# Kernel optimization log

Hardware: AMD Instinct MI355X
Metric: run time of the kernel (lower is better)

Reference implementation:

```python
import jax, jax.numpy as jnp
import numpy as np

INFTY_APPROX = 1e+30
ROTARY_BASE = 10000.0
D_HEAD = 128


def rope(x):
    # x: [B, H, T, D]
    *_, length, width = x.shape
    half = width // 2
    positions = jnp.arange(length)[:, None].astype(x.dtype)          # [T, 1]
    dims = jnp.arange(half).astype(x.dtype)                           # [half]
    ang_freqs = jnp.power(ROTARY_BASE, -dims / half)[None, :]         # [1, half]
    radians = positions * ang_freqs                                   # [T, half]
    cos = jnp.cos(radians)[None, None].astype(x.dtype)                # [1,1,T,half]
    sin = jnp.sin(radians)[None, None].astype(x.dtype)
    even, odd = jnp.split(x, 2, axis=-1)
    r_even = even * cos - odd * sin
    r_odd = even * sin + odd * cos
    return jnp.concatenate([r_even, r_odd], axis=-1)


def setup_inputs() -> dict:
    key = jax.random.key(0)
    ks = jax.random.split(key, 5)
    B, T, M, D = 4, 2048, 1024, D_HEAD
    H = M // D
    x = jax.random.normal(ks[0], (B, T, M), dtype=jnp.float32)
    scale = M ** -0.5
    wq = jax.random.normal(ks[1], (H, M, D), dtype=jnp.float32) * scale
    wk = jax.random.normal(ks[2], (H, M, D), dtype=jnp.float32) * scale
    wv = jax.random.normal(ks[3], (H, M, D), dtype=jnp.float32) * scale
    wo = jax.random.normal(ks[4], (H, D, M), dtype=jnp.float32) * scale
    return {"x": x, "wq": wq, "wk": wk, "wv": wv, "wo": wo}


def reference(x, wq, wk, wv, wo):
    # x: [B, T, M]; w{q,k,v}: [H, M, D]; wo: [H, D, M]
    q = jnp.einsum('bim,hmd->bhid', x, wq)
    k = jnp.einsum('bim,hmd->bhid', x, wk)
    v = jnp.einsum('bim,hmd->bhid', x, wv)
    q = rope(q)
    k = rope(k)
    # NOTE: module scales BOTH q and k by d_head**-0.5 (mup-style 1/d overall)
    mult = jnp.asarray(D_HEAD ** -0.5, dtype=x.dtype)
    s = jnp.einsum('bhid,bhjd->bhij', q * mult, k * mult)
    T = s.shape[-1]
    i = jnp.arange(T)[:, None]
    j = jnp.arange(T)[None, :]
    mask = (i < j).astype(s.dtype)[None, None]  # future positions masked
    s = s - jnp.asarray(INFTY_APPROX, dtype=s.dtype) * mask
    p = jax.nn.softmax(s, axis=-1)
    o = jnp.einsum('bhij,bhjd->bhid', p, v)
    r = jnp.einsum('bhid,hdm->bim', o, wo)
    return r
```

## Files before the change

### kernel.cpp

```cpp
#include <hip/hip_runtime.h>
#include <math.h>


typedef unsigned short u16;
typedef __attribute__((ext_vector_type(8))) short short8;
typedef __attribute__((ext_vector_type(4))) float floatx4;

#define MFMA_B16(a, b, c) __builtin_amdgcn_mfma_f32_16x16x32_bf16((a), (b), (c), 0, 0, 0)

__device__ __forceinline__ void async_cp16(const void* g, void* l) {
  __builtin_amdgcn_global_load_lds(
      (const __attribute__((address_space(1))) unsigned int*)g,
      (__attribute__((address_space(3))) unsigned int*)l, 16, 0, 0);
}

__device__ __forceinline__ u16 f2bf(float f) {
  unsigned u = __float_as_uint(f);
  u += 0x7FFFu + ((u >> 16) & 1u);
  return (u16)(u >> 16);
}

__device__ __forceinline__ unsigned cvt_pk_bf16(float lo, float hi) {
  unsigned r;
  asm("v_cvt_pk_bf16_f32 %0, %1, %2" : "=v"(r) : "v"(lo), "v"(hi));
  return r;
}

__device__ __forceinline__ int swz8(int row, int chunk) { return ((chunk ^ (row & 7)) << 3); }

__global__ void prep_all(const float* __restrict__ x, const float* __restrict__ wq,
                         const float* __restrict__ wk, const float* __restrict__ wv,
                         const float* __restrict__ wo, u16* __restrict__ xb,
                         u16* __restrict__ wT, u16* __restrict__ woT,
                         float2* __restrict__ tab) {
  __shared__ float tile[32][33];
  const int bid = blockIdx.x;
  const int tid = threadIdx.x;

  if (bid < 8192) {
    int idx = (bid * 256 + tid) * 4;
    float4 v = *(const float4*)(x + idx);
    ushort4 o = make_ushort4(f2bf(v.x), f2bf(v.y), f2bf(v.z), f2bf(v.w));
    *(ushort4*)(xb + idx) = o;
  } else if (bid < 11264) {
    int id2 = bid - 8192;
    int z = id2 >> 10;
    int rem = id2 & 1023;
    int by = rem >> 5, bx = rem & 31;
    const float* src = (z == 0) ? wq : (z == 1) ? wk : wv;
    u16* dst = wT + (size_t)z * 1024 * 1024;
    int h = by >> 2, dt = by & 3;
    int m0 = bx * 32, d0 = dt * 32;
    int tx = tid & 31, ty = tid >> 5;
#pragma unroll
    for (int i = 0; i < 4; i++) {
      int r = ty + i * 8;
      tile[r][tx] = src[((size_t)h * 1024 + m0 + r) * 128 + d0 + tx];
    }
    __syncthreads();
#pragma unroll
    for (int i = 0; i < 4; i++) {
      int r = ty + i * 8;
      dst[((size_t)h * 128 + d0 + r) * 1024 + m0 + tx] = f2bf(tile[tx][r]);
    }
  } else if (bid < 12288) {
    int id2 = bid - 11264;
    int by = id2 >> 5, bx = id2 & 31;
    int r0 = by * 32, c0 = bx * 32;
    int tx = tid & 31, ty = tid >> 5;
#pragma unroll
    for (int i = 0; i < 4; i++) {
      int r = ty + i * 8;
      tile[r][tx] = wo[(size_t)(r0 + r) * 1024 + c0 + tx];
    }
    __syncthreads();
#pragma unroll
    for (int i = 0; i < 4; i++) {
      int r = ty + i * 8;
      woT[(size_t)(c0 + r) * 1024 + r0 + tx] = f2bf(tile[tx][r]);
    }
  } else {
    int idx = (bid - 12288) * 256 + tid;
    int t = idx >> 6, d = idx & 63;
    const float c1 = -0.20762050593046015f;
    const float SQ = 0.10616522f;
    float freq = exp2f((float)d * c1);
    float rad = (float)t * freq;
    float s, c;
    sincosf(rad, &s, &c);
    tab[idx] = make_float2(c * SQ, s * SQ);
  }
}

template <int MODE>
__launch_bounds__(256, 3)
__global__ void gemm_bt(const u16* __restrict__ A, const u16* __restrict__ Bt,
                        void* __restrict__ out0, u16* __restrict__ out_k,
                        u16* __restrict__ out_v, const float2* __restrict__ ropetab) {
  __shared__ u16 smem[16384];
  u16* As = smem;
  u16* Bs = smem + 8192;
  const int tid = threadIdx.x;
  const int w = tid >> 6, lane = tid & 63, quad = lane >> 4, l15 = lane & 15;
  const int row0 = blockIdx.x * 128;
  const int by = blockIdx.y;
  const int n0 = by * 128;

  floatx4 acc[2][8] = {};

  for (int kt = 0; kt < 16; ++kt) {
    __syncthreads();
#pragma unroll
    for (int i = 0; i < 4; i++) {
      int cidx = (w * 4 + i) * 64 + lane;
      int r = cidx >> 3, c = cidx & 7, cg = c ^ (r & 7);
      async_cp16(A + (size_t)(row0 + r) * 1024 + kt * 64 + cg * 8, As + (w * 4 + i) * 512);
      async_cp16(Bt + (size_t)(n0 + r) * 1024 + kt * 64 + cg * 8, Bs + (w * 4 + i) * 512);
    }
    __syncthreads();
#pragma unroll
    for (int ks = 0; ks < 2; ks++) {
      short8 af[2];
#pragma unroll
      for (int mi = 0; mi < 2; mi++) {
        int r = w * 32 + mi * 16 + l15;
        af[mi] = *(const short8*)(As + r * 64 + swz8(r, ks * 4 + quad));
      }
#pragma unroll
      for (int ni = 0; ni < 8; ni++) {
        int n = ni * 16 + l15;
        short8 bf = *(const short8*)(Bs + n * 64 + swz8(n, ks * 4 + quad));
        acc[0][ni] = MFMA_B16(af[0], bf, acc[0][ni]);
        acc[1][ni] = MFMA_B16(af[1], bf, acc[1][ni]);
      }
    }
  }
  __syncthreads();

  if (MODE == 0) {
    int sel = by >> 3, h = by & 7;
    if (sel < 2) {
      u16* dst = sel ? out_k : (u16*)out0;
#pragma unroll
      for (int mi = 0; mi < 2; mi++) {
#pragma unroll
        for (int reg = 0; reg < 4; reg++) {
          int row = row0 + w * 32 + mi * 16 + quad * 4 + reg;
          int b = row >> 11, t = row & 2047;
          u16* drow = dst + ((size_t)(b * 8 + h) * 2048 + t) * 128;
#pragma unroll
          for (int ni = 0; ni < 4; ni++) {
            int d = ni * 16 + l15;
            float2 cs = ropetab[t * 64 + d];
            float e = acc[mi][ni][reg], o = acc[mi][ni + 4][reg];
            drow[d] = f2bf(e * cs.x - o * cs.y);
            drow[d + 64] = f2bf(e * cs.y + o * cs.x);
          }
        }
      }
    } else {
#pragma unroll
      for (int mi = 0; mi < 2; mi++) {
#pragma unroll
        for (int reg = 0; reg < 4; reg++) {
          int r = w * 32 + mi * 16 + quad * 4 + reg;
#pragma unroll
          for (int ni = 0; ni < 8; ni++) {
            int col = ni * 16 + l15;
            smem[r * 128 + swz8(r, col >> 3) + (col & 7)] = f2bf(acc[mi][ni][reg]);
          }
        }
      }
      __syncthreads();
      int tl = tid & 127, dg = tid >> 7;
      int row = row0 + tl;
      int b = row >> 11, t = row & 2047;
      int tp = (t & ~31) | ((((t >> 2) & 3) << 3) | (t & 3) | ((t & 16) >> 2));
      u16* vdst = out_v + (size_t)(b * 8 + h) * 128 * 2048;
#pragma unroll
      for (int dd = 0; dd < 64; dd++) {
        int d = dg * 64 + dd;
        u16 val = smem[tl * 128 + swz8(tl, d >> 3) + (d & 7)];
        vdst[(size_t)d * 2048 + tp] = val;
      }
    }
  } else {
    float* outf = (float*)out0;
#pragma unroll
    for (int mi = 0; mi < 2; mi++) {
#pragma unroll
      for (int reg = 0; reg < 4; reg++) {
        int row = row0 + w * 32 + mi * 16 + quad * 4 + reg;
#pragma unroll
        for (int ni = 0; ni < 8; ni++) {
          outf[(size_t)row * 1024 + n0 + ni * 16 + l15] = acc[mi][ni][reg];
        }
      }
    }
  }
}

__device__ __forceinline__ void stage_kv(const u16* kb, const u16* vb, int jt,
                                         u16* Kd, u16* Vd, int w, int lane) {
#pragma unroll
  for (int i = 0; i < 4; i++) {
    int cidx = (w * 4 + i) * 64 + lane;
    int rK = cidx >> 4, cK = cidx & 15, gK = cK ^ (rK & 7);
    async_cp16(kb + (size_t)(jt * 64 + rK) * 128 + gK * 8, Kd + (w * 4 + i) * 512);
    int rV = cidx >> 3, cV = cidx & 7, gV = cV ^ (rV & 7);
    async_cp16(vb + (size_t)rV * 2048 + jt * 64 + gV * 8, Vd + (w * 4 + i) * 512);
  }
}

__device__ __forceinline__ void attn_tile(
    const u16* __restrict__ qb, const u16* __restrict__ kb, const u16* __restrict__ vb,
    u16* __restrict__ O, float* __restrict__ partp, float* __restrict__ plp,
    int qt, int jb, int je, int w, int lane, int quad, int l15,
    u16* smem, int b, int h) {
  const int iw = qt * 128 + w * 32;

  __syncthreads();

  short8 qf[2][4];
#pragma unroll
  for (int mi = 0; mi < 2; mi++) {
    int qrow = iw + mi * 16 + l15;
#pragma unroll
    for (int ks = 0; ks < 4; ks++)
      qf[mi][ks] = *(const short8*)(qb + (size_t)qrow * 128 + ks * 32 + quad * 8);
  }

  short8 onesf;
#pragma unroll
  for (int i = 0; i < 8; i++) onesf[i] = (short)0x3F80;

  floatx4 accO[2][8] = {};
  floatx4 accLs[2] = {};

  stage_kv(kb, vb, jb, smem, smem + 16384, w, lane);

  int cur = 0;
  for (int jt = jb; jt < je; ++jt) {
    __syncthreads();
    if (jt + 1 < je)
      stage_kv(kb, vb, jt + 1, smem + (cur ^ 1) * 8192, smem + 16384 + (cur ^ 1) * 8192, w, lane);

    const u16* Ks = smem + cur * 8192;
    const u16* Vs = smem + 16384 + cur * 8192;
    const int j0 = jt * 64;

    if (j0 <= iw + 31) {
      const bool partial = (j0 + 63 > iw);

      floatx4 sa[4][2] = {};
      __builtin_amdgcn_s_setprio(1);
#pragma unroll
      for (int jj = 0; jj < 4; jj++) {
        const bool ok1 = (j0 + jj * 16 <= iw + 31);
        if (!ok1) continue;
        const bool ok0 = (j0 + jj * 16 <= iw + 15);
#pragma unroll
        for (int ks = 0; ks < 4; ks++) {
          int j = jj * 16 + l15;
          short8 kf = *(const short8*)(Ks + j * 128 + swz8(j, ks * 4 + quad));
          if (ok0) sa[jj][0] = MFMA_B16(kf, qf[0][ks], sa[jj][0]);
          sa[jj][1] = MFMA_B16(kf, qf[1][ks], sa[jj][1]);
        }
      }
      __builtin_amdgcn_s_setprio(0);

      unsigned pk_[2][2][4];
#pragma unroll
      for (int mi = 0; mi < 2; mi++) {
        const int ig = iw + mi * 16 + l15;
#pragma unroll
        for (int jj = 0; jj < 4; jj++) {
          float pv[4];
#pragma unroll
          for (int r = 0; r < 4; r++) {
            float s = sa[jj][mi][r];
            if (partial) {
              int jg = j0 + jj * 16 + quad * 4 + r;
              if (jg > ig) s = -1e30f;
            }
            pv[r] = exp2f(s);
          }
          pk_[mi][jj >> 1][(jj & 1) * 2 + 0] = cvt_pk_bf16(pv[0], pv[1]);
          pk_[mi][jj >> 1][(jj & 1) * 2 + 1] = cvt_pk_bf16(pv[2], pv[3]);
        }
      }

      __builtin_amdgcn_s_setprio(1);
#pragma unroll
      for (int k2 = 0; k2 < 2; k2++) {
        if (k2 == 1 && j0 + 32 > iw + 31) continue;
        union {
          unsigned u[4];
          short8 s8;
        } pa[2];
#pragma unroll
        for (int mi = 0; mi < 2; mi++) {
#pragma unroll
          for (int dw = 0; dw < 4; dw++) pa[mi].u[dw] = pk_[mi][k2][dw];
        }
        accLs[0] = MFMA_B16(pa[0].s8, onesf, accLs[0]);
        accLs[1] = MFMA_B16(pa[1].s8, onesf, accLs[1]);
#pragma unroll
        for (int nt = 0; nt < 8; nt++) {
          int dr = nt * 16 + l15;
          short8 vf = *(const short8*)(Vs + dr * 64 + swz8(dr, k2 * 4 + quad));
          accO[0][nt] = MFMA_B16(pa[0].s8, vf, accO[0][nt]);
          accO[1][nt] = MFMA_B16(pa[1].s8, vf, accO[1][nt]);
        }
      }
      __builtin_amdgcn_s_setprio(0);
    }
    cur ^= 1;
  }

  if (partp == nullptr) {
#pragma unroll
    for (int mi = 0; mi < 2; mi++) {
#pragma unroll
      for (int r = 0; r < 4; r++) {
        float inv = 1.0f / fmaxf(accLs[mi][r], 1e-30f);
        int t = iw + mi * 16 + quad * 4 + r;
#pragma unroll
        for (int nt = 0; nt < 8; nt++) {
          O[(((size_t)b * 2048 + t) * 8 + h) * 128 + nt * 16 + l15] =
              f2bf(accO[mi][nt][r] * inv);
        }
      }
    }
  } else {
#pragma unroll
    for (int mi = 0; mi < 2; mi++) {
#pragma unroll
      for (int r = 0; r < 4; r++) {
        int lrow = w * 32 + mi * 16 + quad * 4 + r;
#pragma unroll
        for (int nt = 0; nt < 8; nt++) {
          partp[lrow * 128 + nt * 16 + l15] = accO[mi][nt][r];
        }
        if (l15 == 0) plp[lrow] = accLs[mi][r];
      }
    }
  }
}

__launch_bounds__(256, 2)
__global__ void flash_attn(const u16* __restrict__ Q, const u16* __restrict__ Kw,
                           const u16* __restrict__ Vw, u16* __restrict__ O,
                           float* __restrict__ part0, float* __restrict__ part1,
                           float* __restrict__ pls) {
  __shared__ u16 smem[32768];

  const int tid = threadIdx.x;
  const int w = tid >> 6, lane = tid & 63, quad = lane >> 4, l15 = lane & 15;

  const int id = (int)blockIdx.x;
  const int half = id >> 8;
  const int sub = id & 255;
  const int bh = sub & 31, p = sub >> 5;

  const u16* qb = Q + (size_t)bh * 2048 * 128;
  const u16* kb = Kw + (size_t)bh * 2048 * 128;
  const u16* vb = Vw + (size_t)bh * 128 * 2048;
  const int b = bh >> 3, h = bh & 7;
  const int bt = 15 - p;

  if (half == 0) {
    attn_tile(qb, kb, vb, O, nullptr, nullptr, p, 0, 2 * p + 2,
              w, lane, quad, l15, smem, b, h);
    attn_tile(qb, kb, vb, O, part0 + (size_t)sub * 16384, pls + (size_t)sub * 128,
              bt, 0, 15 - 2 * p, w, lane, quad, l15, smem, b, h);
  } else {
    attn_tile(qb, kb, vb, O, part1 + (size_t)sub * 16384, pls + (size_t)(256 + sub) * 128,
              bt, 15 - 2 * p, 32 - 2 * p, w, lane, quad, l15, smem, b, h);
  }
}

__global__ void combine(const float* __restrict__ part0, const float* __restrict__ part1,
                        const float* __restrict__ pls, u16* __restrict__ O) {
  __shared__ float ls[128];
  const int job = blockIdx.x;
  const int bh = job & 31, p = job >> 5;
  const int bt = 15 - p;
  const int bb = bh >> 3, h = bh & 7;
  const float* P0 = part0 + (size_t)job * 16384;
  const float* P1 = part1 + (size_t)job * 16384;
  if (threadIdx.x < 128) {
    float s = pls[(size_t)job * 128 + threadIdx.x] + pls[(size_t)(256 + job) * 128 + threadIdx.x];
    ls[threadIdx.x] = 1.0f / fmaxf(s, 1e-30f);
  }
  __syncthreads();
  for (int e = threadIdx.x; e < 16384; e += 256) {
    int row = e >> 7, col = e & 127;
    float v = (P0[e] + P1[e]) * ls[row];
    int t = bt * 128 + row;
    O[(((size_t)bb * 2048 + t) * 8 + h) * 128 + col] = f2bf(v);
  }
}

extern "C" void kernel_launch(void* const* d_in, const int* in_sizes, int n_in,
                              void* d_out, int out_size, void* d_ws, size_t ws_size,
                              hipStream_t stream) {
  const float* x = (const float*)d_in[0];
  const float* wq = (const float*)d_in[1];
  const float* wk = (const float*)d_in[2];
  const float* wv = (const float*)d_in[3];
  const float* wo = (const float*)d_in[4];
  float* out = (float*)d_out;

  char* ws = (char*)d_ws;
  const size_t SZ = 16777216;
  u16* x_bf = (u16*)(ws);
  u16* q_ws = (u16*)(ws + SZ);
  u16* k_ws = (u16*)(ws + 2 * SZ);
  u16* v_ws = (u16*)(ws + 3 * SZ);
  u16* o_ws = (u16*)(ws + 4 * SZ);
  u16* wT = (u16*)(ws + 5 * SZ);
  u16* woT = (u16*)(ws + 5 * SZ + 6291456);
  float2* tab = (float2*)(ws + 5 * SZ + 6291456 + 2097152);
  float* part0 = (float*)x_bf;
  float* part1 = (float*)out;
  float* pls = (float*)((char*)out + 16777216);

  prep_all<<<12800, 256, 0, stream>>>(x, wq, wk, wv, wo, x_bf, wT, woT, tab);
  gemm_bt<0><<<dim3(64, 24), 256, 0, stream>>>(x_bf, wT, q_ws, k_ws, v_ws, tab);
  flash_attn<<<512, 256, 0, stream>>>(q_ws, k_ws, v_ws, o_ws, part0, part1, pls);
  combine<<<256, 256, 0, stream>>>(part0, part1, pls, o_ws);
  gemm_bt<1><<<dim3(64, 8), 256, 0, stream>>>(o_ws, woT, out, nullptr, nullptr, nullptr);
}
```

Baseline: 237.0 us.

## Fuse split-KV combine into flash attention via atomic last-block merge

Removes the separate combine kernel. Each split block writes its partial output and row sums, then increments a per-tile atomic counter, and the block that arrives second merges its register accumulators with the other block's partials to write the final bf16 output. Counters are zeroed in the prep kernel. This saves a kernel launch and one pass that reads and writes the partials. In exchange it adds fences, atomics and extra barriers, and the first tile's leading barrier is moved after the Q loads.

```diff
diff --git a/kernel.cpp b/kernel.cpp
--- a/kernel.cpp
+++ b/kernel.cpp
@@ -32,7 +32,7 @@
                          const float* __restrict__ wk, const float* __restrict__ wv,
                          const float* __restrict__ wo, u16* __restrict__ xb,
                          u16* __restrict__ wT, u16* __restrict__ woT,
-                         float2* __restrict__ tab) {
+                         float2* __restrict__ tab, int* __restrict__ cnt) {
   __shared__ float tile[32][33];
   const int bid = blockIdx.x;
   const int tid = threadIdx.x;
@@ -80,6 +80,7 @@
       woT[(size_t)(c0 + r) * 1024 + r0 + tx] = f2bf(tile[tx][r]);
     }
   } else {
+    if (bid == 12288) cnt[tid] = 0;
     int idx = (bid - 12288) * 256 + tid;
     int t = idx >> 6, d = idx & 63;
     const float c1 = -0.20762050593046015f;
@@ -215,11 +216,11 @@
 __device__ __forceinline__ void attn_tile(
     const u16* __restrict__ qb, const u16* __restrict__ kb, const u16* __restrict__ vb,
     u16* __restrict__ O, float* __restrict__ partp, float* __restrict__ plp,
+    const float* __restrict__ partOther, const float* __restrict__ plOther,
+    int* __restrict__ cntSlot, int* lastflag,
     int qt, int jb, int je, int w, int lane, int quad, int l15,
-    u16* smem, int b, int h) {
+    u16* smem, int b, int h, int tid) {
   const int iw = qt * 128 + w * 32;
-
-  __syncthreads();
 
   short8 qf[2][4];
 #pragma unroll
@@ -229,6 +230,8 @@
     for (int ks = 0; ks < 4; ks++)
       qf[mi][ks] = *(const short8*)(qb + (size_t)qrow * 128 + ks * 32 + quad * 8);
   }
+
+  __syncthreads();
 
   short8 onesf;
 #pragma unroll
@@ -345,6 +348,29 @@
         if (l15 == 0) plp[lrow] = accLs[mi][r];
       }
     }
+    __syncthreads();
+    if (tid == 0) {
+      __threadfence();
+      *lastflag = atomicAdd(cntSlot, 1);
+    }
+    __syncthreads();
+    if (*lastflag == 1) {
+      __threadfence();
+#pragma unroll
+      for (int mi = 0; mi < 2; mi++) {
+#pragma unroll
+        for (int r = 0; r < 4; r++) {
+          int lrow = w * 32 + mi * 16 + quad * 4 + r;
+          float inv = 1.0f / fmaxf(accLs[mi][r] + plOther[lrow], 1e-30f);
+          int t = qt * 128 + lrow;
+#pragma unroll
+          for (int nt = 0; nt < 8; nt++) {
+            float v = accO[mi][nt][r] + partOther[lrow * 128 + nt * 16 + l15];
+            O[(((size_t)b * 2048 + t) * 8 + h) * 128 + nt * 16 + l15] = f2bf(v * inv);
+          }
+        }
+      }
+    }
   }
 }
 
@@ -352,8 +378,9 @@
 __global__ void flash_attn(const u16* __restrict__ Q, const u16* __restrict__ Kw,
                            const u16* __restrict__ Vw, u16* __restrict__ O,
                            float* __restrict__ part0, float* __restrict__ part1,
-                           float* __restrict__ pls) {
+                           float* __restrict__ pls, int* __restrict__ cnt) {
   __shared__ u16 smem[32768];
+  __shared__ int lastflag;
 
   const int tid = threadIdx.x;
   const int w = tid >> 6, lane = tid & 63, quad = lane >> 4, l15 = lane & 15;
@@ -370,35 +397,17 @@
   const int bt = 15 - p;
 
   if (half == 0) {
-    attn_tile(qb, kb, vb, O, nullptr, nullptr, p, 0, 2 * p + 2,
-              w, lane, quad, l15, smem, b, h);
+    attn_tile(qb, kb, vb, O, nullptr, nullptr, nullptr, nullptr, nullptr, &lastflag,
+              p, 0, 2 * p + 2, w, lane, quad, l15, smem, b, h, tid);
     attn_tile(qb, kb, vb, O, part0 + (size_t)sub * 16384, pls + (size_t)sub * 128,
-              bt, 0, 15 - 2 * p, w, lane, quad, l15, smem, b, h);
+              part1 + (size_t)sub * 16384, pls + (size_t)(256 + sub) * 128,
+              cnt + sub, &lastflag,
+              bt, 0, 15 - 2 * p, w, lane, quad, l15, smem, b, h, tid);
   } else {
     attn_tile(qb, kb, vb, O, part1 + (size_t)sub * 16384, pls + (size_t)(256 + sub) * 128,
-              bt, 15 - 2 * p, 32 - 2 * p, w, lane, quad, l15, smem, b, h);
-  }
-}
-
-__global__ void combine(const float* __restrict__ part0, const float* __restrict__ part1,
-                        const float* __restrict__ pls, u16* __restrict__ O) {
-  __shared__ float ls[128];
-  const int job = blockIdx.x;
-  const int bh = job & 31, p = job >> 5;
-  const int bt = 15 - p;
-  const int bb = bh >> 3, h = bh & 7;
-  const float* P0 = part0 + (size_t)job * 16384;
-  const float* P1 = part1 + (size_t)job * 16384;
-  if (threadIdx.x < 128) {
-    float s = pls[(size_t)job * 128 + threadIdx.x] + pls[(size_t)(256 + job) * 128 + threadIdx.x];
-    ls[threadIdx.x] = 1.0f / fmaxf(s, 1e-30f);
-  }
-  __syncthreads();
-  for (int e = threadIdx.x; e < 16384; e += 256) {
-    int row = e >> 7, col = e & 127;
-    float v = (P0[e] + P1[e]) * ls[row];
-    int t = bt * 128 + row;
-    O[(((size_t)bb * 2048 + t) * 8 + h) * 128 + col] = f2bf(v);
+              part0 + (size_t)sub * 16384, pls + (size_t)sub * 128,
+              cnt + sub, &lastflag,
+              bt, 15 - 2 * p, 32 - 2 * p, w, lane, quad, l15, smem, b, h, tid);
   }
 }
 
@@ -422,13 +431,13 @@
   u16* wT = (u16*)(ws + 5 * SZ);
   u16* woT = (u16*)(ws + 5 * SZ + 6291456);
   float2* tab = (float2*)(ws + 5 * SZ + 6291456 + 2097152);
+  int* cnt = (int*)(ws + 5 * SZ + 6291456 + 2097152 + 1048576);
   float* part0 = (float*)x_bf;
   float* part1 = (float*)out;
   float* pls = (float*)((char*)out + 16777216);
 
-  prep_all<<<12800, 256, 0, stream>>>(x, wq, wk, wv, wo, x_bf, wT, woT, tab);
+  prep_all<<<12800, 256, 0, stream>>>(x, wq, wk, wv, wo, x_bf, wT, woT, tab, cnt);
   gemm_bt<0><<<dim3(64, 24), 256, 0, stream>>>(x_bf, wT, q_ws, k_ws, v_ws, tab);
-  flash_attn<<<512, 256, 0, stream>>>(q_ws, k_ws, v_ws, o_ws, part0, part1, pls);
-  combine<<<256, 256, 0, stream>>>(part0, part1, pls, o_ws);
+  flash_attn<<<512, 256, 0, stream>>>(q_ws, k_ws, v_ws, o_ws, part0, part1, pls, cnt);
   gemm_bt<1><<<dim3(64, 8), 256, 0, stream>>>(o_ws, woT, out, nullptr, nullptr, nullptr);
 }
```

Result: slower. 294.4 us (+24.2%).
